# Performance work log

Measured on AMD Instinct MI355X. Metric: run time of the kernel, lower is better.

Reference implementation:

```python
import jax, jax.numpy as jnp
import numpy as np

USER_NUM = 100000
ITEM_NUM = 50000
N_NODES = USER_NUM + ITEM_NUM
NNZ = 4800000
HIDE_DIM = 128
SLOPE = 0.2
EPS = 1e-12  # F.normalize eps


def setup_inputs() -> dict:
    key = jax.random.key(0)
    ks = jax.random.split(key, 9)
    rows = jax.random.randint(ks[0], (NNZ,), 0, N_NODES, dtype=jnp.int32)
    cols = jax.random.randint(ks[1], (NNZ,), 0, N_NODES, dtype=jnp.int32)
    vals = jax.random.uniform(ks[2], (NNZ,), dtype=jnp.float32)
    user_emb = jax.random.normal(ks[3], (USER_NUM, HIDE_DIM), dtype=jnp.float32) * 0.1
    item_emb = jax.random.normal(ks[4], (ITEM_NUM, HIDE_DIM), dtype=jnp.float32) * 0.1
    u_w0 = jax.random.normal(ks[5], (HIDE_DIM, HIDE_DIM), dtype=jnp.float32) * 0.05
    v_w0 = jax.random.normal(ks[6], (HIDE_DIM, HIDE_DIM), dtype=jnp.float32) * 0.05
    u_w1 = jax.random.normal(ks[7], (HIDE_DIM, HIDE_DIM), dtype=jnp.float32) * 0.05
    v_w1 = jax.random.normal(ks[8], (HIDE_DIM, HIDE_DIM), dtype=jnp.float32) * 0.05
    return {"rows": rows, "cols": cols, "vals": vals,
            "user_emb": user_emb, "item_emb": item_emb,
            "u_w0": u_w0, "v_w0": v_w0, "u_w1": u_w1, "v_w1": v_w1}


def _spmm(rows, cols, vals, feat):
    # sparse [N,N] @ dense [N,D] via gather + segment_sum
    gathered = vals[:, None] * feat[cols]            # [nnz, D]
    return jax.ops.segment_sum(gathered, rows, num_segments=N_NODES)


def _gcn_layer(rows, cols, vals, u_feat, i_feat, u_w, v_w):
    feat = jnp.concatenate([u_feat @ u_w, i_feat @ v_w], axis=0)  # [N, D]
    return jax.nn.leaky_relu(_spmm(rows, cols, vals, feat), negative_slope=SLOPE)


def _l2norm(x):
    n = jnp.sqrt(jnp.sum(x * x, axis=1, keepdims=True))
    return x / jnp.maximum(n, EPS)


def reference(rows, cols, vals, user_emb, item_emb, u_w0, v_w0, u_w1, v_w1):
    all_u = [user_emb]
    all_i = [item_emb]
    # layer 0 consumes raw embeddings
    emb = _gcn_layer(rows, cols, vals, user_emb, item_emb, u_w0, v_w0)
    norm = _l2norm(emb)
    all_u.append(norm[:USER_NUM]); all_i.append(norm[USER_NUM:])
    # layer 1 consumes UNNORMALIZED previous layer output (as in the torch code)
    emb = _gcn_layer(rows, cols, vals, emb[:USER_NUM], emb[USER_NUM:], u_w1, v_w1)
    norm = _l2norm(emb)
    all_u.append(norm[:USER_NUM]); all_i.append(norm[USER_NUM:])
    user_embedding = jnp.concatenate(all_u, axis=1)  # [userNum, 3*D]
    item_embedding = jnp.concatenate(all_i, axis=1)  # [itemNum, 3*D]
    return (user_embedding, item_embedding)
```

## Files before the change

kernel.cpp:

```cpp
#include <hip/hip_runtime.h>

#define D 128
#define OUTD 384
#define SLOPE 0.2f
#define BSH 7
#define BROWS 128
#define MAXNB 2048
#define FCAP 4736
#define SPAN 8192
#define SCT 512
#define FTH 512
#define NSMAX 1025

typedef __attribute__((ext_vector_type(8))) short bf16x8;
typedef __attribute__((ext_vector_type(4))) float f32x4;

__device__ __forceinline__ unsigned f2bf(float f) {
    unsigned u = __float_as_uint(f);
    return (u + 0x7FFFu + ((u >> 16) & 1u)) >> 16;
}

__device__ __forceinline__ void nt_store_f4(float4 v, float* p) {
    f32x4 t = {v.x, v.y, v.z, v.w};
    __builtin_nontemporal_store(t, (f32x4*)p);
}

__global__ __launch_bounds__(256) void wt_prep(const float* __restrict__ W0,
                                               const float* __restrict__ W1,
                                               const float* __restrict__ W2,
                                               const float* __restrict__ W3,
                                               unsigned short* __restrict__ wt) {
    const float* Ws[4] = {W0, W1, W2, W3};
    const float* W = Ws[blockIdx.x];
    unsigned short* o = wt + (size_t)blockIdx.x * 16384;
    for (int i = threadIdx.x; i < 16384; i += 256) {
        int k = i >> 7, n = i & 127;
        o[(size_t)n * 128 + k] = (unsigned short)f2bf(W[(size_t)k * 128 + n]);
    }
}

#define GR 64
#define APAD 136
__global__ __launch_bounds__(256) void gemm_mfma(const float* __restrict__ in, int pitch,
                                                 const unsigned short* __restrict__ Wt,
                                                 unsigned short* __restrict__ featb,
                                                 const float* __restrict__ rowscale,
                                                 float* __restrict__ rawout,
                                                 int nrows) {
    __shared__ unsigned short sA[GR * APAD];
    __shared__ unsigned short sW[128 * APAD];
    int tid = threadIdx.x;
    int row0 = blockIdx.x * GR;
    int nr = min(GR, nrows - row0);

    for (int i = tid; i < GR * 32; i += 256) {
        int r = i >> 5, c4 = (i & 31) * 4;
        unsigned lo = 0, hi = 0;
        if (r < nr) {
            float4 t = *(const float4*)&in[(size_t)(row0 + r) * pitch + c4];
            if (rawout)
                nt_store_f4(t, &rawout[(size_t)(row0 + r) * OUTD + c4]);
            if (rowscale) {
                float s = rowscale[row0 + r];
                t.x *= s; t.y *= s; t.z *= s; t.w *= s;
            }
            lo = f2bf(t.x) | (f2bf(t.y) << 16);
            hi = f2bf(t.z) | (f2bf(t.w) << 16);
        }
        uint2 pk = {lo, hi};
        *(uint2*)&sA[r * APAD + c4] = pk;
    }
    for (int i = tid; i < 128 * 16; i += 256) {
        int n = i >> 4, k8 = (i & 15) * 8;
        *(uint4*)&sW[n * APAD + k8] = *(const uint4*)&Wt[(size_t)n * 128 + k8];
    }
    __syncthreads();

    int l  = tid & 63;
    int w  = tid >> 6;
    int lr = l & 15;
    int lk = (l >> 4) * 8;

    f32x4 acc[8];
#pragma unroll
    for (int t = 0; t < 8; ++t) acc[t] = (f32x4){0.f, 0.f, 0.f, 0.f};

#pragma unroll
    for (int k0 = 0; k0 < 128; k0 += 32) {
        bf16x8 af = *(const bf16x8*)&sA[(16 * w + lr) * APAD + k0 + lk];
#pragma unroll
        for (int t = 0; t < 8; ++t) {
            bf16x8 bf = *(const bf16x8*)&sW[(t * 16 + lr) * APAD + k0 + lk];
            acc[t] = __builtin_amdgcn_mfma_f32_16x16x32_bf16(af, bf, acc[t], 0, 0, 0);
        }
    }

    int rbase = 16 * w + (l >> 4) * 4;
#pragma unroll
    for (int t = 0; t < 8; ++t) {
#pragma unroll
        for (int q = 0; q < 4; ++q) {
            int r = rbase + q;
            if (r < nr)
                featb[(size_t)(row0 + r) * D + t * 16 + lr] = (unsigned short)f2bf(acc[t][q]);
        }
    }
}

__global__ __launch_bounds__(SCT) void seg_scatter(const int* __restrict__ rows,
                                                   const int* __restrict__ cols,
                                                   const float* __restrict__ vals,
                                                   uint2* __restrict__ etmp,
                                                   int* __restrict__ offmat,
                                                   int nnz, int NB) {
    __shared__ int hist[MAXNB];
    __shared__ int wsum[8];
    int tid = threadIdx.x;
    int sgm = blockIdx.x;
    int lo  = sgm * SPAN;
    int hi  = min(lo + SPAN, nnz);
    if (lo >= nnz) return;

    for (int i = tid; i < NB; i += SCT) hist[i] = 0;
    __syncthreads();

    int4 r4[4];
#pragma unroll
    for (int q = 0; q < 4; ++q) {
        int e = lo + (q * SCT + tid) * 4;
        if (e + 3 < hi) {
            r4[q] = *(const int4*)&rows[e];
            atomicAdd(&hist[r4[q].x >> BSH], 1);
            atomicAdd(&hist[r4[q].y >> BSH], 1);
            atomicAdd(&hist[r4[q].z >> BSH], 1);
            atomicAdd(&hist[r4[q].w >> BSH], 1);
        } else {
            int t0 = (e + 0 < hi) ? rows[e + 0] : -1;
            int t1 = (e + 1 < hi) ? rows[e + 1] : -1;
            int t2 = (e + 2 < hi) ? rows[e + 2] : -1;
            int t3 = (e + 3 < hi) ? rows[e + 3] : -1;
            if (t0 >= 0) atomicAdd(&hist[t0 >> BSH], 1);
            if (t1 >= 0) atomicAdd(&hist[t1 >> BSH], 1);
            if (t2 >= 0) atomicAdd(&hist[t2 >> BSH], 1);
            if (t3 >= 0) atomicAdd(&hist[t3 >> BSH], 1);
            r4[q] = make_int4(t0, t1, t2, t3);
        }
    }
    __syncthreads();

    int per = (NB + SCT - 1) / SCT;
    int base = tid * per;
    int lv[4];
    int lsum = 0;
#pragma unroll
    for (int k = 0; k < 4; ++k) {
        int idx = base + k;
        int v = (k < per && idx < NB) ? hist[idx] : 0;
        lv[k] = v; lsum += v;
    }
    int lane = tid & 63, wid = tid >> 6;
    int incl = lsum;
#pragma unroll
    for (int off = 1; off < 64; off <<= 1) {
        int t = __shfl_up(incl, off);
        if (lane >= off) incl += t;
    }
    if (lane == 63) wsum[wid] = incl;
    __syncthreads();
    int woff = 0;
    for (int w = 0; w < wid; ++w) woff += wsum[w];
    int run = woff + incl - lsum;
    __syncthreads();
    int rowbase = sgm * (NB + 1);
#pragma unroll
    for (int k = 0; k < 4; ++k) {
        int idx = base + k;
        if (k < per && idx < NB) {
            int c = lv[k];
            hist[idx] = run;
            offmat[rowbase + idx] = run;
            run += c;
        }
    }
    if (NB - 1 >= base && NB - 1 < base + per)
        offmat[rowbase + NB] = run;
    __syncthreads();

#define SEMIT(r, c, v)                                                             \
    {                                                                              \
        int pos_ = atomicAdd(&hist[(r) >> BSH], 1);                                \
        etmp[lo + pos_] = make_uint2(((unsigned)((r) & (BROWS - 1)) << 18) |       \
                                     (unsigned)(c), __float_as_uint(v));           \
    }
#pragma unroll
    for (int q = 0; q < 4; ++q) {
        int e = lo + (q * SCT + tid) * 4;
        if (e + 3 < hi) {
            int4   c4 = *(const int4*)&cols[e];
            float4 v4 = *(const float4*)&vals[e];
            SEMIT(r4[q].x, c4.x, v4.x);
            SEMIT(r4[q].y, c4.y, v4.y);
            SEMIT(r4[q].z, c4.z, v4.z);
            SEMIT(r4[q].w, c4.w, v4.w);
        } else {
            int rr0 = r4[q].x, rr1 = r4[q].y, rr2 = r4[q].z, rr3 = r4[q].w;
            if (rr0 >= 0) { SEMIT(rr0, cols[e + 0], vals[e + 0]); }
            if (rr1 >= 0) { SEMIT(rr1, cols[e + 1], vals[e + 1]); }
            if (rr2 >= 0) { SEMIT(rr2, cols[e + 2], vals[e + 2]); }
            if (rr3 >= 0) { SEMIT(rr3, cols[e + 3], vals[e + 3]); }
        }
    }
}

__global__ __launch_bounds__(FTH) void seg_finalize(const uint2* __restrict__ etmp,
                                                    const int* __restrict__ offmat,
                                                    uint2* __restrict__ esort,
                                                    int* __restrict__ row_start,
                                                    int* __restrict__ rend,
                                                    int N, int NB, int NS, int cap) {
    __shared__ uint2 ed[FCAP];
    __shared__ int srcoff[NSMAX], dstoff[NSMAX];
    __shared__ int rcnt[BROWS], rbase[BROWS];
    __shared__ int wsum[8];
    __shared__ int tot;
    int b   = blockIdx.x;
    int tid = threadIdx.x;
    int lane = tid & 63, wid = tid >> 6;
    if (tid < BROWS) rcnt[tid] = 0;

    int per = (NS + FTH - 1) / FTH;
    int base = tid * per;
    int lo0[2], ll[2];
    int lsum = 0;
#pragma unroll
    for (int k = 0; k < 2; ++k) {
        int s = base + k;
        int o0 = 0, l = 0;
        if (k < per && s < NS) {
            int rb = s * (NB + 1) + b;
            o0 = offmat[rb];
            l  = offmat[rb + 1] - o0;
        }
        lo0[k] = o0; ll[k] = l; lsum += l;
    }
    int incl = lsum;
#pragma unroll
    for (int off = 1; off < 64; off <<= 1) {
        int t = __shfl_up(incl, off);
        if (lane >= off) incl += t;
    }
    if (lane == 63) wsum[wid] = incl;
    __syncthreads();
    int woff = 0;
    for (int w = 0; w < wid; ++w) woff += wsum[w];
    int run = woff + incl - lsum;
#pragma unroll
    for (int k = 0; k < 2; ++k) {
        int s = base + k;
        if (k < per && s < NS) {
            srcoff[s] = lo0[k];
            dstoff[s] = run;
            run += ll[k];
        }
    }
    if (NS - 1 >= base && NS - 1 < base + per) {
        tot = min(run, cap);
        dstoff[NS] = run;
    }
    __syncthreads();

    int tl = tot;
    for (int d = tid; d < tl; d += FTH) {
        int s0 = 0, s1 = NS;
        while (s1 - s0 > 1) {
            int mid = (s0 + s1) >> 1;
            if (dstoff[mid] <= d) s0 = mid; else s1 = mid;
        }
        int src = s0 * SPAN + srcoff[s0] + (d - dstoff[s0]);
        uint2 t = etmp[src];
        ed[d] = t;
        atomicAdd(&rcnt[t.x >> 18], 1);
    }
    __syncthreads();

    int c = (tid < BROWS) ? rcnt[tid] : 0;
    int incl2 = c;
#pragma unroll
    for (int off = 1; off < 64; off <<= 1) {
        int t = __shfl_up(incl2, off);
        if (lane >= off) incl2 += t;
    }
    if (tid < BROWS && lane == 63) wsum[wid] = incl2;
    __syncthreads();
    if (tid < BROWS) {
        int woff2 = (wid == 1) ? wsum[0] : 0;
        int excl = woff2 + incl2 - c;
        rbase[tid] = b * cap + excl;
        int row = b * BROWS + tid;
        if (row < N) { row_start[row] = b * cap + excl; rend[row] = b * cap + excl + c; }
    }
    __syncthreads();

    for (int d = tid; d < tl; d += FTH) {
        uint2 t = ed[d];
        int pos = atomicAdd(&rbase[t.x >> 18], 1);
        esort[pos] = make_uint2(t.x & 0x3FFFFu, t.y);
    }
}

#define ACCQ(vbits, g)                                             \
    {                                                              \
        float v = __uint_as_float(vbits);                          \
        acc0.x += v * __uint_as_float((g).x << 16);                \
        acc0.y += v * __uint_as_float((g).x & 0xFFFF0000u);        \
        acc0.z += v * __uint_as_float((g).y << 16);                \
        acc0.w += v * __uint_as_float((g).y & 0xFFFF0000u);        \
        acc1.x += v * __uint_as_float((g).z << 16);                \
        acc1.y += v * __uint_as_float((g).z & 0xFFFF0000u);        \
        acc1.z += v * __uint_as_float((g).w << 16);                \
        acc1.w += v * __uint_as_float((g).w & 0xFFFF0000u);        \
    }

__global__ __launch_bounds__(256) void spmm_csr4(const uint2* __restrict__ ep,
                                                 const int* __restrict__ rstart,
                                                 const int* __restrict__ rend,
                                                 const unsigned short* __restrict__ featb,
                                                 float* __restrict__ out,
                                                 float* __restrict__ nsave,
                                                 int col_off, int N) {
    int row  = blockIdx.x * 4 + (threadIdx.x >> 6);
    if (row >= N) return;
    int lane = threadIdx.x & 63;
    int j = lane & 15;
    int h = lane >> 4;
    int s = rstart[row], e = rend[row];

    float4 acc0 = {0.f, 0.f, 0.f, 0.f};
    float4 acc1 = {0.f, 0.f, 0.f, 0.f};
    int i = s;
    for (; i + 16 <= e; i += 16) {
        uint2 eA = ep[i + h];
        uint2 eB = ep[i + 4 + h];
        uint2 eC = ep[i + 8 + h];
        uint2 eD = ep[i + 12 + h];
        uint4 gA = *(const uint4*)&featb[(size_t)eA.x * D + j * 8];
        uint4 gB = *(const uint4*)&featb[(size_t)eB.x * D + j * 8];
        uint4 gC = *(const uint4*)&featb[(size_t)eC.x * D + j * 8];
        uint4 gD = *(const uint4*)&featb[(size_t)eD.x * D + j * 8];
        ACCQ(eA.y, gA);
        ACCQ(eB.y, gB);
        ACCQ(eC.y, gC);
        ACCQ(eD.y, gD);
    }
    for (; i + 8 <= e; i += 8) {
        uint2 eA = ep[i + h];
        uint2 eB = ep[i + 4 + h];
        uint4 gA = *(const uint4*)&featb[(size_t)eA.x * D + j * 8];
        uint4 gB = *(const uint4*)&featb[(size_t)eB.x * D + j * 8];
        ACCQ(eA.y, gA);
        ACCQ(eB.y, gB);
    }
    for (; i < e; i += 4) {
        int idx = i + h;
        uint2 ev = make_uint2(0u, 0u);
        if (idx < e) ev = ep[idx];
        uint4 g = *(const uint4*)&featb[(size_t)ev.x * D + j * 8];
        ACCQ(ev.y, g);
    }

#pragma unroll
    for (int m = 16; m <= 32; m <<= 1) {
        acc0.x += __shfl_xor(acc0.x, m);
        acc0.y += __shfl_xor(acc0.y, m);
        acc0.z += __shfl_xor(acc0.z, m);
        acc0.w += __shfl_xor(acc0.w, m);
        acc1.x += __shfl_xor(acc1.x, m);
        acc1.y += __shfl_xor(acc1.y, m);
        acc1.z += __shfl_xor(acc1.z, m);
        acc1.w += __shfl_xor(acc1.w, m);
    }

    acc0.x = (acc0.x > 0.f) ? acc0.x : SLOPE * acc0.x;
    acc0.y = (acc0.y > 0.f) ? acc0.y : SLOPE * acc0.y;
    acc0.z = (acc0.z > 0.f) ? acc0.z : SLOPE * acc0.z;
    acc0.w = (acc0.w > 0.f) ? acc0.w : SLOPE * acc0.w;
    acc1.x = (acc1.x > 0.f) ? acc1.x : SLOPE * acc1.x;
    acc1.y = (acc1.y > 0.f) ? acc1.y : SLOPE * acc1.y;
    acc1.z = (acc1.z > 0.f) ? acc1.z : SLOPE * acc1.z;
    acc1.w = (acc1.w > 0.f) ? acc1.w : SLOPE * acc1.w;

    float ss = acc0.x * acc0.x + acc0.y * acc0.y + acc0.z * acc0.z + acc0.w * acc0.w
             + acc1.x * acc1.x + acc1.y * acc1.y + acc1.z * acc1.z + acc1.w * acc1.w;
#pragma unroll
    for (int m = 8; m >= 1; m >>= 1) ss += __shfl_xor(ss, m);
    float nm = fmaxf(sqrtf(ss), 1e-12f);
    float sc = 1.0f / nm;

    if (nsave && lane == 0) nsave[row] = nm;
    if (h == 0) {
        float* dst = &out[(size_t)row * OUTD + col_off + j * 8];
        float4 o0 = {acc0.x * sc, acc0.y * sc, acc0.z * sc, acc0.w * sc};
        float4 o1 = {acc1.x * sc, acc1.y * sc, acc1.z * sc, acc1.w * sc};
        *(float4*)&dst[0] = o0;
        *(float4*)&dst[4] = o1;
    }
}

extern "C" void kernel_launch(void* const* d_in, const int* in_sizes, int n_in,
                              void* d_out, int out_size, void* d_ws, size_t ws_size,
                              hipStream_t stream) {
    const int*   rows = (const int*)d_in[0];
    const int*   cols = (const int*)d_in[1];
    const float* vals = (const float*)d_in[2];
    const float* ue   = (const float*)d_in[3];
    const float* ie   = (const float*)d_in[4];
    const float* uw0  = (const float*)d_in[5];
    const float* vw0  = (const float*)d_in[6];
    const float* uw1  = (const float*)d_in[7];
    const float* vw1  = (const float*)d_in[8];
    float* out = (float*)d_out;

    int nnz = in_sizes[0];
    int U   = in_sizes[3] / D;
    int I   = in_sizes[4] / D;
    int N   = U + I;
    int NB  = (N + BROWS - 1) >> BSH;
    int NS  = (nnz + SPAN - 1) / SPAN;

    int avg = nnz / NB;
    int cap = avg + avg / 8 + 64;
    if (cap > FCAP) cap = FCAP;

    char* p = (char*)d_ws;
    size_t unionSz = (size_t)N * D * 2;
    if ((size_t)nnz * 8 > unionSz) unionSz = (size_t)nnz * 8;
    unsigned short* featb = (unsigned short*)p;
    uint2*          etmp  = (uint2*)p;           p += unionSz;
    uint2* esort          = (uint2*)p;           p += (size_t)NB * cap * 8;
    int* row_start        = (int*)p;             p += (size_t)N * 4;
    int* rend             = (int*)p;             p += (size_t)N * 4;
    float* nsave          = (float*)p;           p += (size_t)N * 4;
    p = (char*)(((size_t)p + 63) & ~(size_t)63);
    int* offmat           = (int*)p;             p += (size_t)NS * (NB + 1) * 4;
    p = (char*)(((size_t)p + 63) & ~(size_t)63);
    unsigned short* wtbuf = (unsigned short*)p;  p += (size_t)4 * 16384 * 2;

    int row_blocks = (N + 3) / 4;
    int gu = (U + GR - 1) / GR;
    int gi = (I + GR - 1) / GR;

    wt_prep<<<4, 256, 0, stream>>>(uw0, vw0, uw1, vw1, wtbuf);

    seg_scatter<<<NS, SCT, 0, stream>>>(rows, cols, vals, etmp, offmat, nnz, NB);
    seg_finalize<<<NB, FTH, 0, stream>>>(etmp, offmat, esort, row_start, rend,
                                         N, NB, NS, cap);

    gemm_mfma<<<gu, 256, 0, stream>>>(ue, D, wtbuf, featb, nullptr, out, U);
    gemm_mfma<<<gi, 256, 0, stream>>>(ie, D, wtbuf + 16384, featb + (size_t)U * D,
                                      nullptr, out + (size_t)U * OUTD, I);
    spmm_csr4<<<row_blocks, 256, 0, stream>>>(esort, row_start, rend, featb, out,
                                              nsave, D, N);

    gemm_mfma<<<gu, 256, 0, stream>>>(out + D, OUTD, wtbuf + 2 * 16384, featb,
                                      nsave, nullptr, U);
    gemm_mfma<<<gi, 256, 0, stream>>>(out + (size_t)U * OUTD + D, OUTD, wtbuf + 3 * 16384,
                                      featb + (size_t)U * D, nsave + U, nullptr, I);
    spmm_csr4<<<row_blocks, 256, 0, stream>>>(esort, row_start, rend, featb, out,
                                              nullptr, 2 * D, N);
}
```

Before: 581.4 us.

## Fuse scatter, weight prep and layer-0 GEMMs into one launch

Merges the edge-bucketing scatter, the layer-1 weight transpose and the two layer-0 GEMMs into a single heterogeneous kernel dispatched by block index. Layer-0 GEMMs now convert the raw fp32 weights to transposed bf16 in LDS themselves. To allow this, featb and etmp get separate workspace regions instead of aliasing, with the old sequential path kept as a fallback when the workspace is too small. The GEMM also moves to 512 threads, with each wave computing half the output columns. The goal is fewer launches and overlapping independent phases, at the cost of more workspace and higher LDS use per block in the fused kernel.

```diff
diff --git a/kernel.cpp b/kernel.cpp
--- a/kernel.cpp
+++ b/kernel.cpp
@@ -8,9 +8,11 @@
 #define MAXNB 2048
 #define FCAP 4736
 #define SPAN 8192
-#define SCT 512
 #define FTH 512
 #define NSMAX 1025
+#define GR 64
+#define APAD 136
+#define GEMM_LDS (GR * APAD * 2 + 128 * APAD * 2)
 
 typedef __attribute__((ext_vector_type(8))) short bf16x8;
 typedef __attribute__((ext_vector_type(4))) float f32x4;
@@ -25,35 +27,28 @@
     __builtin_nontemporal_store(t, (f32x4*)p);
 }
 
-__global__ __launch_bounds__(256) void wt_prep(const float* __restrict__ W0,
-                                               const float* __restrict__ W1,
-                                               const float* __restrict__ W2,
-                                               const float* __restrict__ W3,
-                                               unsigned short* __restrict__ wt) {
-    const float* Ws[4] = {W0, W1, W2, W3};
-    const float* W = Ws[blockIdx.x];
-    unsigned short* o = wt + (size_t)blockIdx.x * 16384;
-    for (int i = threadIdx.x; i < 16384; i += 256) {
+
+__device__ void dev_wtprep(const float* __restrict__ W, unsigned short* __restrict__ o) {
+    for (int i = threadIdx.x; i < 16384; i += 512) {
         int k = i >> 7, n = i & 127;
         o[(size_t)n * 128 + k] = (unsigned short)f2bf(W[(size_t)k * 128 + n]);
     }
 }
 
-#define GR 64
-#define APAD 136
-__global__ __launch_bounds__(256) void gemm_mfma(const float* __restrict__ in, int pitch,
-                                                 const unsigned short* __restrict__ Wt,
-                                                 unsigned short* __restrict__ featb,
-                                                 const float* __restrict__ rowscale,
-                                                 float* __restrict__ rawout,
-                                                 int nrows) {
-    __shared__ unsigned short sA[GR * APAD];
-    __shared__ unsigned short sW[128 * APAD];
+__device__ void dev_gemm(char* smem, const float* __restrict__ in, int pitch,
+                         const unsigned short* __restrict__ Wt,
+                         const float* __restrict__ Wraw,
+                         unsigned short* __restrict__ featb,
+                         const float* __restrict__ rowscale,
+                         float* __restrict__ rawout,
+                         int nrows, int blk) {
+    unsigned short* sA = (unsigned short*)smem;
+    unsigned short* sW = sA + GR * APAD;
     int tid = threadIdx.x;
-    int row0 = blockIdx.x * GR;
+    int row0 = blk * GR;
     int nr = min(GR, nrows - row0);
 
-    for (int i = tid; i < GR * 32; i += 256) {
+    for (int i = tid; i < GR * 32; i += 512) {
         int r = i >> 5, c4 = (i & 31) * 4;
         unsigned lo = 0, hi = 0;
         if (r < nr) {
@@ -70,64 +65,78 @@
         uint2 pk = {lo, hi};
         *(uint2*)&sA[r * APAD + c4] = pk;
     }
-    for (int i = tid; i < 128 * 16; i += 256) {
-        int n = i >> 4, k8 = (i & 15) * 8;
-        *(uint4*)&sW[n * APAD + k8] = *(const uint4*)&Wt[(size_t)n * 128 + k8];
+    if (Wt) {
+        for (int i = tid; i < 128 * 16; i += 512) {
+            int n = i >> 4, k8 = (i & 15) * 8;
+            *(uint4*)&sW[n * APAD + k8] = *(const uint4*)&Wt[(size_t)n * 128 + k8];
+        }
+    } else {
+        for (int i = tid; i < 128 * 32; i += 512) {
+            int k = i >> 5, c4 = (i & 31) * 4;
+            float4 t = *(const float4*)&Wraw[(size_t)k * 128 + c4];
+            sW[(c4 + 0) * APAD + k] = (unsigned short)f2bf(t.x);
+            sW[(c4 + 1) * APAD + k] = (unsigned short)f2bf(t.y);
+            sW[(c4 + 2) * APAD + k] = (unsigned short)f2bf(t.z);
+            sW[(c4 + 3) * APAD + k] = (unsigned short)f2bf(t.w);
+        }
     }
     __syncthreads();
 
     int l  = tid & 63;
-    int w  = tid >> 6;
+    int w8 = tid >> 6;
+    int rowTile = w8 >> 1;
+    int colHalf = w8 & 1;
     int lr = l & 15;
     int lk = (l >> 4) * 8;
 
-    f32x4 acc[8];
-#pragma unroll
-    for (int t = 0; t < 8; ++t) acc[t] = (f32x4){0.f, 0.f, 0.f, 0.f};
+    f32x4 acc[4];
+#pragma unroll
+    for (int t = 0; t < 4; ++t) acc[t] = (f32x4){0.f, 0.f, 0.f, 0.f};
 
 #pragma unroll
     for (int k0 = 0; k0 < 128; k0 += 32) {
-        bf16x8 af = *(const bf16x8*)&sA[(16 * w + lr) * APAD + k0 + lk];
-#pragma unroll
-        for (int t = 0; t < 8; ++t) {
-            bf16x8 bf = *(const bf16x8*)&sW[(t * 16 + lr) * APAD + k0 + lk];
+        bf16x8 af = *(const bf16x8*)&sA[(16 * rowTile + lr) * APAD + k0 + lk];
+#pragma unroll
+        for (int t = 0; t < 4; ++t) {
+            bf16x8 bf = *(const bf16x8*)&sW[((colHalf * 4 + t) * 16 + lr) * APAD + k0 + lk];
             acc[t] = __builtin_amdgcn_mfma_f32_16x16x32_bf16(af, bf, acc[t], 0, 0, 0);
         }
     }
 
-    int rbase = 16 * w + (l >> 4) * 4;
-#pragma unroll
-    for (int t = 0; t < 8; ++t) {
+    int rbase = 16 * rowTile + (l >> 4) * 4;
+#pragma unroll
+    for (int t = 0; t < 4; ++t) {
 #pragma unroll
         for (int q = 0; q < 4; ++q) {
             int r = rbase + q;
             if (r < nr)
-                featb[(size_t)(row0 + r) * D + t * 16 + lr] = (unsigned short)f2bf(acc[t][q]);
-        }
-    }
-}
-
-__global__ __launch_bounds__(SCT) void seg_scatter(const int* __restrict__ rows,
-                                                   const int* __restrict__ cols,
-                                                   const float* __restrict__ vals,
-                                                   uint2* __restrict__ etmp,
-                                                   int* __restrict__ offmat,
-                                                   int nnz, int NB) {
-    __shared__ int hist[MAXNB];
-    __shared__ int wsum[8];
+                featb[(size_t)(row0 + r) * D + (colHalf * 4 + t) * 16 + lr] =
+                    (unsigned short)f2bf(acc[t][q]);
+        }
+    }
+}
+
+__device__ void dev_scatter(char* smem,
+                            const int* __restrict__ rows,
+                            const int* __restrict__ cols,
+                            const float* __restrict__ vals,
+                            uint2* __restrict__ etmp,
+                            int* __restrict__ offmat,
+                            int nnz, int NB, int sgm) {
+    int* hist = (int*)smem;
+    int* wsum = hist + MAXNB;
     int tid = threadIdx.x;
-    int sgm = blockIdx.x;
     int lo  = sgm * SPAN;
     int hi  = min(lo + SPAN, nnz);
     if (lo >= nnz) return;
 
-    for (int i = tid; i < NB; i += SCT) hist[i] = 0;
+    for (int i = tid; i < NB; i += 512) hist[i] = 0;
     __syncthreads();
 
     int4 r4[4];
 #pragma unroll
     for (int q = 0; q < 4; ++q) {
-        int e = lo + (q * SCT + tid) * 4;
+        int e = lo + (q * 512 + tid) * 4;
         if (e + 3 < hi) {
             r4[q] = *(const int4*)&rows[e];
             atomicAdd(&hist[r4[q].x >> BSH], 1);
@@ -148,7 +157,7 @@
     }
     __syncthreads();
 
-    int per = (NB + SCT - 1) / SCT;
+    int per = (NB + 511) / 512;
     int base = tid * per;
     int lv[4];
     int lsum = 0;
@@ -194,7 +203,7 @@
     }
 #pragma unroll
     for (int q = 0; q < 4; ++q) {
-        int e = lo + (q * SCT + tid) * 4;
+        int e = lo + (q * 512 + tid) * 4;
         if (e + 3 < hi) {
             int4   c4 = *(const int4*)&cols[e];
             float4 v4 = *(const float4*)&vals[e];
@@ -210,6 +219,53 @@
             if (rr3 >= 0) { SEMIT(rr3, cols[e + 3], vals[e + 3]); }
         }
     }
+#undef SEMIT
+}
+
+__global__ __launch_bounds__(512) void k_phase1(const int* rows, const int* cols,
+                                                const float* vals, uint2* etmp,
+                                                int* offmat, int nnz, int NB, int NS,
+                                                const float* ue, const float* ie,
+                                                const float* uw0, const float* vw0,
+                                                const float* uw1, const float* vw1,
+                                                unsigned short* wtbuf,
+                                                unsigned short* featb, float* out,
+                                                int U, int I, int gu) {
+    extern __shared__ char smem[];
+    int b = blockIdx.x;
+    if (b < NS) {
+        dev_scatter(smem, rows, cols, vals, etmp, offmat, nnz, NB, b);
+    } else if (b < NS + 2) {
+        dev_wtprep((b - NS == 0) ? uw1 : vw1, wtbuf + (size_t)(2 + (b - NS)) * 16384);
+    } else if (b < NS + 2 + gu) {
+        dev_gemm(smem, ue, D, nullptr, uw0, featb, nullptr, out, U, b - NS - 2);
+    } else {
+        dev_gemm(smem, ie, D, nullptr, vw0, featb + (size_t)U * D, nullptr,
+                 out + (size_t)U * OUTD, I, b - NS - 2 - gu);
+    }
+}
+
+__global__ __launch_bounds__(512) void k_gemm(const float* in, int pitch,
+                                              const unsigned short* Wt,
+                                              unsigned short* featb,
+                                              const float* rowscale, float* rawout,
+                                              int nrows) {
+    __shared__ char smem[GEMM_LDS];
+    dev_gemm(smem, in, pitch, Wt, nullptr, featb, rowscale, rawout, nrows, blockIdx.x);
+}
+
+__global__ __launch_bounds__(512) void k_wtprep4(const float* W0, const float* W1,
+                                                 const float* W2, const float* W3,
+                                                 unsigned short* wt) {
+    const float* Ws[4] = {W0, W1, W2, W3};
+    dev_wtprep(Ws[blockIdx.x], wt + (size_t)blockIdx.x * 16384);
+}
+
+__global__ __launch_bounds__(512) void k_scatter(const int* rows, const int* cols,
+                                                 const float* vals, uint2* etmp,
+                                                 int* offmat, int nnz, int NB) {
+    extern __shared__ char smem[];
+    dev_scatter(smem, rows, cols, vals, etmp, offmat, nnz, NB, blockIdx.x);
 }
 
 __global__ __launch_bounds__(FTH) void seg_finalize(const uint2* __restrict__ etmp,
@@ -431,40 +487,75 @@
     int cap = avg + avg / 8 + 64;
     if (cap > FCAP) cap = FCAP;
 
-    char* p = (char*)d_ws;
-    size_t unionSz = (size_t)N * D * 2;
-    if ((size_t)nnz * 8 > unionSz) unionSz = (size_t)nnz * 8;
-    unsigned short* featb = (unsigned short*)p;
-    uint2*          etmp  = (uint2*)p;           p += unionSz;
-    uint2* esort          = (uint2*)p;           p += (size_t)NB * cap * 8;
-    int* row_start        = (int*)p;             p += (size_t)N * 4;
-    int* rend             = (int*)p;             p += (size_t)N * 4;
-    float* nsave          = (float*)p;           p += (size_t)N * 4;
-    p = (char*)(((size_t)p + 63) & ~(size_t)63);
-    int* offmat           = (int*)p;             p += (size_t)NS * (NB + 1) * 4;
-    p = (char*)(((size_t)p + 63) & ~(size_t)63);
-    unsigned short* wtbuf = (unsigned short*)p;  p += (size_t)4 * 16384 * 2;
-
     int row_blocks = (N + 3) / 4;
     int gu = (U + GR - 1) / GR;
     int gi = (I + GR - 1) / GR;
 
-    wt_prep<<<4, 256, 0, stream>>>(uw0, vw0, uw1, vw1, wtbuf);
-
-    seg_scatter<<<NS, SCT, 0, stream>>>(rows, cols, vals, etmp, offmat, nnz, NB);
-    seg_finalize<<<NB, FTH, 0, stream>>>(etmp, offmat, esort, row_start, rend,
-                                         N, NB, NS, cap);
-
-    gemm_mfma<<<gu, 256, 0, stream>>>(ue, D, wtbuf, featb, nullptr, out, U);
-    gemm_mfma<<<gi, 256, 0, stream>>>(ie, D, wtbuf + 16384, featb + (size_t)U * D,
-                                      nullptr, out + (size_t)U * OUTD, I);
-    spmm_csr4<<<row_blocks, 256, 0, stream>>>(esort, row_start, rend, featb, out,
-                                              nsave, D, N);
-
-    gemm_mfma<<<gu, 256, 0, stream>>>(out + D, OUTD, wtbuf + 2 * 16384, featb,
-                                      nsave, nullptr, U);
-    gemm_mfma<<<gi, 256, 0, stream>>>(out + (size_t)U * OUTD + D, OUTD, wtbuf + 3 * 16384,
-                                      featb + (size_t)U * D, nsave + U, nullptr, I);
-    spmm_csr4<<<row_blocks, 256, 0, stream>>>(esort, row_start, rend, featb, out,
-                                              nullptr, 2 * D, N);
-}
+    size_t featbSz = (size_t)N * D * 2;
+    size_t etmpSz  = (size_t)NS * SPAN * 8;
+    size_t esortSz = (size_t)NB * cap * 8;
+    size_t miscSz  = (size_t)N * 12 + (size_t)NS * (NB + 1) * 4 + 4 * 16384 * 2 + 256;
+    size_t needFused = featbSz + etmpSz + esortSz + miscSz;
+
+    if (ws_size >= needFused) {
+        char* p = (char*)d_ws;
+        unsigned short* featb = (unsigned short*)p;  p += featbSz;
+        uint2* etmp           = (uint2*)p;           p += etmpSz;
+        uint2* esort          = (uint2*)p;           p += esortSz;
+        int* row_start        = (int*)p;             p += (size_t)N * 4;
+        int* rend             = (int*)p;             p += (size_t)N * 4;
+        float* nsave          = (float*)p;           p += (size_t)N * 4;
+        p = (char*)(((size_t)p + 63) & ~(size_t)63);
+        int* offmat           = (int*)p;             p += (size_t)NS * (NB + 1) * 4;
+        p = (char*)(((size_t)p + 63) & ~(size_t)63);
+        unsigned short* wtbuf = (unsigned short*)p;
+
+        k_phase1<<<NS + 2 + gu + gi, 512, GEMM_LDS, stream>>>(
+            rows, cols, vals, etmp, offmat, nnz, NB, NS,
+            ue, ie, uw0, vw0, uw1, vw1, wtbuf, featb, out, U, I, gu);
+
+        seg_finalize<<<NB, FTH, 0, stream>>>(etmp, offmat, esort, row_start, rend,
+                                             N, NB, NS, cap);
+        spmm_csr4<<<row_blocks, 256, 0, stream>>>(esort, row_start, rend, featb, out,
+                                                  nsave, D, N);
+
+        k_gemm<<<gu, 512, 0, stream>>>(out + D, OUTD, wtbuf + 2 * 16384, featb,
+                                       nsave, nullptr, U);
+        k_gemm<<<gi, 512, 0, stream>>>(out + (size_t)U * OUTD + D, OUTD, wtbuf + 3 * 16384,
+                                       featb + (size_t)U * D, nsave + U, nullptr, I);
+        spmm_csr4<<<row_blocks, 256, 0, stream>>>(esort, row_start, rend, featb, out,
+                                                  nullptr, 2 * D, N);
+    } else {
+        char* p = (char*)d_ws;
+        size_t unionSz = featbSz > etmpSz ? featbSz : etmpSz;
+        unsigned short* featb = (unsigned short*)p;
+        uint2*          etmp  = (uint2*)p;           p += unionSz;
+        uint2* esort          = (uint2*)p;           p += esortSz;
+        int* row_start        = (int*)p;             p += (size_t)N * 4;
+        int* rend             = (int*)p;             p += (size_t)N * 4;
+        float* nsave          = (float*)p;           p += (size_t)N * 4;
+        p = (char*)(((size_t)p + 63) & ~(size_t)63);
+        int* offmat           = (int*)p;             p += (size_t)NS * (NB + 1) * 4;
+        p = (char*)(((size_t)p + 63) & ~(size_t)63);
+        unsigned short* wtbuf = (unsigned short*)p;
+
+        k_wtprep4<<<4, 512, 0, stream>>>(uw0, vw0, uw1, vw1, wtbuf);
+        k_scatter<<<NS, 512, MAXNB * 4 + 64, stream>>>(rows, cols, vals, etmp, offmat,
+                                                       nnz, NB);
+        seg_finalize<<<NB, FTH, 0, stream>>>(etmp, offmat, esort, row_start, rend,
+                                             N, NB, NS, cap);
+
+        k_gemm<<<gu, 512, 0, stream>>>(ue, D, wtbuf, featb, nullptr, out, U);
+        k_gemm<<<gi, 512, 0, stream>>>(ie, D, wtbuf + 16384, featb + (size_t)U * D,
+                                       nullptr, out + (size_t)U * OUTD, I);
+        spmm_csr4<<<row_blocks, 256, 0, stream>>>(esort, row_start, rend, featb, out,
+                                                  nsave, D, N);
+
+        k_gemm<<<gu, 512, 0, stream>>>(out + D, OUTD, wtbuf + 2 * 16384, featb,
+                                       nsave, nullptr, U);
+        k_gemm<<<gi, 512, 0, stream>>>(out + (size_t)U * OUTD + D, OUTD, wtbuf + 3 * 16384,
+                                       featb + (size_t)U * D, nsave + U, nullptr, I);
+        spmm_csr4<<<row_blocks, 256, 0, stream>>>(esort, row_start, rend, featb, out,
+                                                  nullptr, 2 * D, N);
+    }
+}
```

Measured after the change: 528.8 us. -9.0%, faster.
